# Optimization experiments

Hardware: AMD Instinct MI355X
Metric: run time of the kernel (lower is better)

## Reference

```python
import jax, jax.numpy as jnp
import numpy as np

N, D_IN, D_OUT = 2048, 256, 64
ALPHA = 0.2  # LeakyReLU slope
LN_EPS = 1e-5


def setup_inputs() -> dict:
    key = jax.random.key(0)
    ks = jax.random.split(key, 8)
    features = jax.random.normal(ks[0], (N, D_IN), dtype=jnp.float32)
    adj = jax.random.randint(ks[1], (N, N), 0, 2, dtype=jnp.int32)
    adj = adj.at[jnp.arange(N), jnp.arange(N)].set(1)  # self-loops: no all-masked rows
    s_in = 1.0 / np.sqrt(D_IN)
    s_out = 1.0 / np.sqrt(D_OUT)
    phi_w = jax.random.uniform(ks[2], (D_OUT, D_IN), jnp.float32, -s_in, s_in)
    phi_b = jax.random.uniform(ks[3], (D_OUT,), jnp.float32, -s_in, s_in)
    mu_w = jax.random.uniform(ks[4], (D_OUT,), jnp.float32, -s_out, s_out)
    mu_b = jax.random.uniform(ks[5], (), jnp.float32, -s_out, s_out)
    ln_g = jnp.ones((D_OUT,), jnp.float32)
    ln_b = jnp.zeros((D_OUT,), jnp.float32)
    return {"features": features, "adj": adj, "phi_w": phi_w, "phi_b": phi_b,
            "ln_g": ln_g, "ln_b": ln_b, "mu_w": mu_w, "mu_b": mu_b}


def _layernorm(x, g, b):
    mu = jnp.mean(x, axis=-1, keepdims=True)
    var = jnp.mean(jnp.square(x - mu), axis=-1, keepdims=True)
    return (x - mu) * jax.lax.rsqrt(var + LN_EPS) * g + b


def reference(features, adj, phi_w, phi_b, ln_g, ln_b, mu_w, mu_b):
    h = features @ phi_w.T + phi_b           # [N, D_OUT]
    h = _layernorm(h, ln_g, ln_b)
    # v2 path: scores[i,j,:] = h[i] + h[j]; e = mu(scores)
    scores = h[:, None, :] + h[None, :, :]   # [N, N, D_OUT]
    e = jnp.einsum('ijd,d->ij', scores, mu_w) + mu_b  # [N, N]
    e = jax.nn.leaky_relu(e, ALPHA)          # activation applied after if/else
    e = jnp.where(adj == 0, -jnp.inf, e)
    a = jax.nn.softmax(e, axis=1)            # dropout p=0 -> identity
    return jax.nn.elu(a @ h)                 # [N, D_OUT]
```

## Files before the change

kernel.cpp:

```cpp
#include <hip/hip_runtime.h>
#include <hip/hip_bf16.h>

#define N_ROWS 2048
#define D_IN   256
#define D_OUT  64
#define JSLAB  8
#define ALPHA  0.2f
#define LN_EPS 1e-5f

typedef __attribute__((ext_vector_type(4))) float f32x4;
typedef __attribute__((ext_vector_type(8))) short s16x8;

static __device__ __forceinline__ unsigned short f2bf(float x) {
    unsigned u = __float_as_uint(x);
    unsigned r = (u + 0x7FFFu + ((u >> 16) & 1u)) >> 16;
    return (unsigned short)r;
}
static __device__ __forceinline__ float bf2f(unsigned short u) {
    return __uint_as_float(((unsigned)u) << 16);
}

__global__ __launch_bounds__(256) void k1_h_s(
    const float* __restrict__ F, const float* __restrict__ phiW,
    const float* __restrict__ phiB, const float* __restrict__ lnG,
    const float* __restrict__ lnB, const float* __restrict__ muW,
    float* __restrict__ s_out, unsigned short* __restrict__ HhiT,
    unsigned short* __restrict__ HloT)
{
    __shared__ f32x4 phiS[64 * 64];
    __shared__ unsigned short Thi[64][8];
    __shared__ unsigned short Tlo[64][8];

    const int tid  = threadIdx.x;
    const int w    = tid >> 6;
    const int lane = tid & 63;
    const int i_base = blockIdx.x * 8;
    const int r0 = i_base + w * 2;

    const f32x4* phiW4 = (const f32x4*)phiW;
    const f32x4* F4    = (const f32x4*)F;

    #pragma unroll
    for (int t = 0; t < 16; ++t) {
        int idx = tid + t * 256;
        int d = idx >> 6, g = idx & 63;
        phiS[(d << 6) | (g ^ (d & 7))] = phiW4[idx];
    }
    __syncthreads();

    float acc[2] = {0.f, 0.f};
    for (int g = 0; g < 64; ++g) {
        f32x4 p = phiS[(lane << 6) | (g ^ (lane & 7))];
        #pragma unroll
        for (int rr = 0; rr < 2; ++rr) {
            f32x4 f = F4[(r0 + rr) * 64 + g];
            acc[rr] += p.x * f.x + p.y * f.y + p.z * f.z + p.w * f.w;
        }
    }

    const float pb = phiB[lane], gg = lnG[lane], bb = lnB[lane], mw = muW[lane];

    #pragma unroll
    for (int rr = 0; rr < 2; ++rr) {
        float h = acc[rr] + pb;
        float m = h;
        #pragma unroll
        for (int off = 32; off >= 1; off >>= 1) m += __shfl_xor(m, off);
        m *= (1.f / 64.f);
        float c = h - m;
        float v = c * c;
        #pragma unroll
        for (int off = 32; off >= 1; off >>= 1) v += __shfl_xor(v, off);
        v *= (1.f / 64.f);
        float hn = c * rsqrtf(v + LN_EPS) * gg + bb;
        float sp = hn * mw;
        #pragma unroll
        for (int off = 32; off >= 1; off >>= 1) sp += __shfl_xor(sp, off);
        if (lane == 0) s_out[r0 + rr] = sp;
        unsigned short hi = f2bf(hn);
        unsigned short lo = f2bf(hn - bf2f(hi));
        Thi[lane][w * 2 + rr] = hi;
        Tlo[lane][w * 2 + rr] = lo;
    }
    __syncthreads();
    if (tid < 128) {
        int d = tid >> 1, half = tid & 1;
        ushort4 vh = *(const ushort4*)&Thi[d][half * 4];
        *(ushort4*)&HhiT[d * N_ROWS + i_base + half * 4] = vh;
        ushort4 vl = *(const ushort4*)&Tlo[d][half * 4];
        *(ushort4*)&HloT[d * N_ROWS + i_base + half * 4] = vl;
    }
}

__global__ __launch_bounds__(256) void k2_attn(
    const int* __restrict__ adj, const float* __restrict__ s,
    const unsigned short* __restrict__ HhiT, const unsigned short* __restrict__ HloT,
    const float* __restrict__ muB,
    float* __restrict__ num_p, float* __restrict__ l_p)
{
    const int tid  = threadIdx.x;
    const int w    = tid >> 6;
    const int lane = tid & 63;
    const int stripe = blockIdx.x >> 3;
    const int slab   = blockIdx.x & (JSLAB - 1);
    const int i0 = stripe * 16;
    const int jb = slab * 256 + w * 64;
    const float mub = muB[0];

    __shared__ __align__(16) unsigned short Wt[4][16][72];
    __shared__ f32x4 cN[4][4][64];
    __shared__ f32x4 cL[4][64];

    const int rsel = lane & 15;
    const int rsub = lane >> 4;

    f32x4 accN[4];
    f32x4 accL;
    #pragma unroll
    for (int nb = 0; nb < 4; ++nb) { accN[nb][0]=0.f; accN[nb][1]=0.f; accN[nb][2]=0.f; accN[nb][3]=0.f; }
    accL[0]=0.f; accL[1]=0.f; accL[2]=0.f; accL[3]=0.f;

    s16x8 ones;
    #pragma unroll
    for (int e = 0; e < 8; ++e) ones[e] = (short)0x3F80;

    const float4 sj4 = ((const float4*)s)[(jb >> 2) + rsel];
    const int4* adj4 = (const int4*)adj;
    #pragma unroll
    for (int r4 = 0; r4 < 4; ++r4) {
        const int row = r4 * 4 + rsub;
        const int i = i0 + row;
        const float si = s[i];
        int4 a = adj4[(size_t)i * (N_ROWS / 4) + (jb >> 2) + rsel];
        ushort4 pk;
        {
            float z = si + sj4.x + mub; float e = z > 0.f ? z : ALPHA * z;
            pk.x = a.x ? f2bf(__expf(e)) : 0;
        }{
            float z = si + sj4.y + mub; float e = z > 0.f ? z : ALPHA * z;
            pk.y = a.y ? f2bf(__expf(e)) : 0;
        }{
            float z = si + sj4.z + mub; float e = z > 0.f ? z : ALPHA * z;
            pk.z = a.z ? f2bf(__expf(e)) : 0;
        }{
            float z = si + sj4.w + mub; float e = z > 0.f ? z : ALPHA * z;
            pk.w = a.w ? f2bf(__expf(e)) : 0;
        }
        *(ushort4*)&Wt[w][row][rsel * 4] = pk;
    }

    s16x8 a0 = *(const s16x8*)&Wt[w][rsel][rsub * 8];
    s16x8 a1 = *(const s16x8*)&Wt[w][rsel][32 + rsub * 8];

    accL = __builtin_amdgcn_mfma_f32_16x16x32_bf16(a0, ones, accL, 0, 0, 0);
    accL = __builtin_amdgcn_mfma_f32_16x16x32_bf16(a1, ones, accL, 0, 0, 0);
    #pragma unroll
    for (int nb = 0; nb < 4; ++nb) {
        const unsigned short* hr = HhiT + (size_t)(nb * 16 + rsel) * N_ROWS + jb + rsub * 8;
        s16x8 b0 = *(const s16x8*)hr;
        s16x8 b1 = *(const s16x8*)(hr + 32);
        accN[nb] = __builtin_amdgcn_mfma_f32_16x16x32_bf16(a0, b0, accN[nb], 0, 0, 0);
        accN[nb] = __builtin_amdgcn_mfma_f32_16x16x32_bf16(a1, b1, accN[nb], 0, 0, 0);
        const unsigned short* lr = HloT + (size_t)(nb * 16 + rsel) * N_ROWS + jb + rsub * 8;
        s16x8 c0 = *(const s16x8*)lr;
        s16x8 c1 = *(const s16x8*)(lr + 32);
        accN[nb] = __builtin_amdgcn_mfma_f32_16x16x32_bf16(a0, c0, accN[nb], 0, 0, 0);
        accN[nb] = __builtin_amdgcn_mfma_f32_16x16x32_bf16(a1, c1, accN[nb], 0, 0, 0);
    }

    #pragma unroll
    for (int nb = 0; nb < 4; ++nb) cN[w][nb][lane] = accN[nb];
    cL[w][lane] = accL;
    __syncthreads();

    {
        f32x4 n = cN[0][w][lane] + cN[1][w][lane] + cN[2][w][lane] + cN[3][w][lane];
        float* np = num_p + (size_t)slab * (N_ROWS * D_OUT);
        #pragma unroll
        for (int r = 0; r < 4; ++r)
            np[(i0 + rsub * 4 + r) * D_OUT + w * 16 + rsel] = n[r];
    }
    if (w == 0) {
        f32x4 l = cL[0][lane] + cL[1][lane] + cL[2][lane] + cL[3][lane];
        if (rsel == 0) {
            #pragma unroll
            for (int r = 0; r < 4; ++r)
                l_p[slab * N_ROWS + i0 + rsub * 4 + r] = l[r];
        }
    }
}

__global__ __launch_bounds__(256) void k3_combine(
    const float* __restrict__ num_p, const float* __restrict__ l_p,
    float* __restrict__ out)
{
    const int g = blockIdx.x * 256 + threadIdx.x;
    const int i = g >> 6;
    float num = 0.f, l = 0.f;
    #pragma unroll
    for (int js = 0; js < JSLAB; ++js) {
        num += num_p[(size_t)js * (N_ROWS * D_OUT) + g];
        l   += l_p[js * N_ROWS + i];
    }
    const float o = num / l;
    out[g] = o > 0.f ? o : expm1f(o);
}

extern "C" void kernel_launch(void* const* d_in, const int* in_sizes, int n_in,
                              void* d_out, int out_size, void* d_ws, size_t ws_size,
                              hipStream_t stream)
{
    const float* F    = (const float*)d_in[0];
    const int*   adj  = (const int*)d_in[1];
    const float* phiW = (const float*)d_in[2];
    const float* phiB = (const float*)d_in[3];
    const float* lnG  = (const float*)d_in[4];
    const float* lnB  = (const float*)d_in[5];
    const float* muW  = (const float*)d_in[6];
    const float* muB  = (const float*)d_in[7];
    float* out = (float*)d_out;

    float* ws   = (float*)d_ws;
    float* s    = ws;
    float* l_p  = ws + N_ROWS;
    float* numP = l_p + (size_t)JSLAB * N_ROWS;
    unsigned short* HhiT = (unsigned short*)(numP + (size_t)JSLAB * N_ROWS * D_OUT);
    unsigned short* HloT = HhiT + (size_t)D_OUT * N_ROWS;

    k1_h_s<<<dim3(N_ROWS / 8), dim3(256), 0, stream>>>(F, phiW, phiB, lnG, lnB, muW,
                                                       s, HhiT, HloT);
    k2_attn<<<dim3((N_ROWS / 16) * JSLAB), dim3(256), 0, stream>>>(adj, s, HhiT, HloT, muB,
                                                                   numP, l_p);
    k3_combine<<<dim3((N_ROWS * D_OUT) / 256), dim3(256), 0, stream>>>(numP, l_p, out);
}
```

Baseline: 27.13 us.

## Fuse three kernels into one persistent kernel with grid barrier and finisher combine

Merges the projection/LayerNorm kernel, the attention slab kernel and the combine kernel into one 512-block launch. A global atomic grid barrier separates phase one from phase two, and a per-stripe atomic counter lets the last block for each stripe do the final normalize and ELU. The aim is to remove two kernel launch gaps and the separate combine pass. In exchange it adds a memset launch and spin-wait barrier overhead, and it relies on all 512 blocks being co-resident (launch bounds of 2 blocks per CU); otherwise the barrier deadlocks.

```diff
diff --git a/kernel.cpp b/kernel.cpp
--- a/kernel.cpp
+++ b/kernel.cpp
@@ -5,6 +5,7 @@
 #define D_IN   256
 #define D_OUT  64
 #define JSLAB  8
+#define NBLK   512
 #define ALPHA  0.2f
 #define LN_EPS 1e-5f
 
@@ -20,49 +21,61 @@
     return __uint_as_float(((unsigned)u) << 16);
 }
 
-__global__ __launch_bounds__(256) void k1_h_s(
-    const float* __restrict__ F, const float* __restrict__ phiW,
-    const float* __restrict__ phiB, const float* __restrict__ lnG,
-    const float* __restrict__ lnB, const float* __restrict__ muW,
-    float* __restrict__ s_out, unsigned short* __restrict__ HhiT,
-    unsigned short* __restrict__ HloT)
+__global__ __launch_bounds__(256, 2) void fused_gat(
+    const float* __restrict__ F, const int* __restrict__ adj,
+    const float* __restrict__ phiW, const float* __restrict__ phiB,
+    const float* __restrict__ lnG, const float* __restrict__ lnB,
+    const float* __restrict__ muW, const float* __restrict__ muB,
+    int* __restrict__ bar,
+    float* __restrict__ s_buf, float* __restrict__ l_p,
+    float* __restrict__ numP, unsigned short* __restrict__ HhiT,
+    unsigned short* __restrict__ HloT, float* __restrict__ out)
 {
-    __shared__ f32x4 phiS[64 * 64];
-    __shared__ unsigned short Thi[64][8];
-    __shared__ unsigned short Tlo[64][8];
+    __shared__ union {
+        struct {
+            f32x4 phiS[64 * 32];
+            unsigned short Thi[64][4];
+            unsigned short Tlo[64][4];
+        } p1;
+        struct {
+            unsigned short Wt[4][16][72];
+            f32x4 cN[4][4][64];
+            f32x4 cL[4][64];
+        } p2;
+    } sm;
+    __shared__ int finisher;
 
     const int tid  = threadIdx.x;
     const int w    = tid >> 6;
     const int lane = tid & 63;
-    const int i_base = blockIdx.x * 8;
-    const int r0 = i_base + w * 2;
-
-    const f32x4* phiW4 = (const f32x4*)phiW;
-    const f32x4* F4    = (const f32x4*)F;
-
-    #pragma unroll
-    for (int t = 0; t < 16; ++t) {
-        int idx = tid + t * 256;
-        int d = idx >> 6, g = idx & 63;
-        phiS[(d << 6) | (g ^ (d & 7))] = phiW4[idx];
-    }
-    __syncthreads();
-
-    float acc[2] = {0.f, 0.f};
-    for (int g = 0; g < 64; ++g) {
-        f32x4 p = phiS[(lane << 6) | (g ^ (lane & 7))];
-        #pragma unroll
-        for (int rr = 0; rr < 2; ++rr) {
-            f32x4 f = F4[(r0 + rr) * 64 + g];
-            acc[rr] += p.x * f.x + p.y * f.y + p.z * f.z + p.w * f.w;
-        }
-    }
-
-    const float pb = phiB[lane], gg = lnG[lane], bb = lnB[lane], mw = muW[lane];
-
-    #pragma unroll
-    for (int rr = 0; rr < 2; ++rr) {
-        float h = acc[rr] + pb;
+    const int bid  = blockIdx.x;
+
+    {
+        const int r = bid * 4 + w;
+        const f32x4* phiW4 = (const f32x4*)phiW;
+        const f32x4* F4    = (const f32x4*)F;
+
+        float acc0 = 0.f, acc1 = 0.f;
+        for (int half = 0; half < 2; ++half) {
+            __syncthreads();
+            #pragma unroll
+            for (int t = 0; t < 8; ++t) {
+                int idx = tid + t * 256;
+                int d = idx >> 5, g = idx & 31;
+                sm.p1.phiS[(d << 5) | (g ^ (d & 7))] = phiW4[d * 64 + half * 32 + g];
+            }
+            __syncthreads();
+            #pragma unroll
+            for (int g = 0; g < 32; ++g) {
+                f32x4 p = sm.p1.phiS[(lane << 5) | (g ^ (lane & 7))];
+                f32x4 f = F4[r * 64 + half * 32 + g];
+                float d0 = p.x * f.x + p.y * f.y + p.z * f.z + p.w * f.w;
+                if (g & 1) acc1 += d0; else acc0 += d0;
+            }
+        }
+
+        const float pb = phiB[lane], gg = lnG[lane], bb = lnB[lane], mw = muW[lane];
+        float h = acc0 + acc1 + pb;
         float m = h;
         #pragma unroll
         for (int off = 32; off >= 1; off >>= 1) m += __shfl_xor(m, off);
@@ -76,134 +89,143 @@
         float sp = hn * mw;
         #pragma unroll
         for (int off = 32; off >= 1; off >>= 1) sp += __shfl_xor(sp, off);
-        if (lane == 0) s_out[r0 + rr] = sp;
+        if (lane == 0) s_buf[r] = sp;
         unsigned short hi = f2bf(hn);
         unsigned short lo = f2bf(hn - bf2f(hi));
-        Thi[lane][w * 2 + rr] = hi;
-        Tlo[lane][w * 2 + rr] = lo;
-    }
-    __syncthreads();
-    if (tid < 128) {
-        int d = tid >> 1, half = tid & 1;
-        ushort4 vh = *(const ushort4*)&Thi[d][half * 4];
-        *(ushort4*)&HhiT[d * N_ROWS + i_base + half * 4] = vh;
-        ushort4 vl = *(const ushort4*)&Tlo[d][half * 4];
-        *(ushort4*)&HloT[d * N_ROWS + i_base + half * 4] = vl;
-    }
-}
-
-__global__ __launch_bounds__(256) void k2_attn(
-    const int* __restrict__ adj, const float* __restrict__ s,
-    const unsigned short* __restrict__ HhiT, const unsigned short* __restrict__ HloT,
-    const float* __restrict__ muB,
-    float* __restrict__ num_p, float* __restrict__ l_p)
-{
-    const int tid  = threadIdx.x;
-    const int w    = tid >> 6;
-    const int lane = tid & 63;
-    const int stripe = blockIdx.x >> 3;
-    const int slab   = blockIdx.x & (JSLAB - 1);
+        sm.p1.Thi[lane][w] = hi;
+        sm.p1.Tlo[lane][w] = lo;
+        __syncthreads();
+        if (tid < 64) {
+            *(ushort4*)&HhiT[tid * N_ROWS + bid * 4] = *(const ushort4*)&sm.p1.Thi[tid][0];
+        } else if (tid < 128) {
+            int d = tid - 64;
+            *(ushort4*)&HloT[d * N_ROWS + bid * 4] = *(const ushort4*)&sm.p1.Tlo[d][0];
+        }
+    }
+
+    __syncthreads();
+    if (tid == 0) {
+        __threadfence();
+        atomicAdd(&bar[0], 1);
+        while (atomicAdd(&bar[0], 0) < NBLK) __builtin_amdgcn_s_sleep(1);
+        __threadfence();
+    }
+    __syncthreads();
+
+    const int stripe = bid >> 2;
     const int i0 = stripe * 16;
-    const int jb = slab * 256 + w * 64;
     const float mub = muB[0];
-
-    __shared__ __align__(16) unsigned short Wt[4][16][72];
-    __shared__ f32x4 cN[4][4][64];
-    __shared__ f32x4 cL[4][64];
-
     const int rsel = lane & 15;
     const int rsub = lane >> 4;
-
-    f32x4 accN[4];
-    f32x4 accL;
-    #pragma unroll
-    for (int nb = 0; nb < 4; ++nb) { accN[nb][0]=0.f; accN[nb][1]=0.f; accN[nb][2]=0.f; accN[nb][3]=0.f; }
-    accL[0]=0.f; accL[1]=0.f; accL[2]=0.f; accL[3]=0.f;
 
     s16x8 ones;
     #pragma unroll
     for (int e = 0; e < 8; ++e) ones[e] = (short)0x3F80;
 
-    const float4 sj4 = ((const float4*)s)[(jb >> 2) + rsel];
-    const int4* adj4 = (const int4*)adj;
     #pragma unroll
-    for (int r4 = 0; r4 < 4; ++r4) {
-        const int row = r4 * 4 + rsub;
-        const int i = i0 + row;
-        const float si = s[i];
-        int4 a = adj4[(size_t)i * (N_ROWS / 4) + (jb >> 2) + rsel];
-        ushort4 pk;
+    for (int t = 0; t < 2; ++t) {
+        const int slab = (bid * 2 + t) & 7;
+        const int jb = slab * 256 + w * 64;
+
+        f32x4 accN[4];
+        f32x4 accL;
+        #pragma unroll
+        for (int nb = 0; nb < 4; ++nb) { accN[nb][0]=0.f; accN[nb][1]=0.f; accN[nb][2]=0.f; accN[nb][3]=0.f; }
+        accL[0]=0.f; accL[1]=0.f; accL[2]=0.f; accL[3]=0.f;
+
+        __syncthreads();
+
+        const float4 sj4 = ((const float4*)s_buf)[(jb >> 2) + rsel];
+        const int4* adj4 = (const int4*)adj;
+        #pragma unroll
+        for (int r4 = 0; r4 < 4; ++r4) {
+            const int row = r4 * 4 + rsub;
+            const int i = i0 + row;
+            const float si = s_buf[i];
+            int4 a = adj4[(size_t)i * (N_ROWS / 4) + (jb >> 2) + rsel];
+            ushort4 pk;
+            { float z = si + sj4.x + mub; float e = z > 0.f ? z : ALPHA * z; pk.x = a.x ? f2bf(__expf(e)) : 0; }
+            { float z = si + sj4.y + mub; float e = z > 0.f ? z : ALPHA * z; pk.y = a.y ? f2bf(__expf(e)) : 0; }
+            { float z = si + sj4.z + mub; float e = z > 0.f ? z : ALPHA * z; pk.z = a.z ? f2bf(__expf(e)) : 0; }
+            { float z = si + sj4.w + mub; float e = z > 0.f ? z : ALPHA * z; pk.w = a.w ? f2bf(__expf(e)) : 0; }
+            *(ushort4*)&sm.p2.Wt[w][row][rsel * 4] = pk;
+        }
+
+        s16x8 a0 = *(const s16x8*)&sm.p2.Wt[w][rsel][rsub * 8];
+        s16x8 a1 = *(const s16x8*)&sm.p2.Wt[w][rsel][32 + rsub * 8];
+
+        accL = __builtin_amdgcn_mfma_f32_16x16x32_bf16(a0, ones, accL, 0, 0, 0);
+        accL = __builtin_amdgcn_mfma_f32_16x16x32_bf16(a1, ones, accL, 0, 0, 0);
+        #pragma unroll
+        for (int nb = 0; nb < 4; ++nb) {
+            const unsigned short* hr = HhiT + (size_t)(nb * 16 + rsel) * N_ROWS + jb + rsub * 8;
+            s16x8 b0 = *(const s16x8*)hr;
+            s16x8 b1 = *(const s16x8*)(hr + 32);
+            accN[nb] = __builtin_amdgcn_mfma_f32_16x16x32_bf16(a0, b0, accN[nb], 0, 0, 0);
+            accN[nb] = __builtin_amdgcn_mfma_f32_16x16x32_bf16(a1, b1, accN[nb], 0, 0, 0);
+            const unsigned short* lr = HloT + (size_t)(nb * 16 + rsel) * N_ROWS + jb + rsub * 8;
+            s16x8 c0 = *(const s16x8*)lr;
+            s16x8 c1 = *(const s16x8*)(lr + 32);
+            accN[nb] = __builtin_amdgcn_mfma_f32_16x16x32_bf16(a0, c0, accN[nb], 0, 0, 0);
+            accN[nb] = __builtin_amdgcn_mfma_f32_16x16x32_bf16(a1, c1, accN[nb], 0, 0, 0);
+        }
+
+        #pragma unroll
+        for (int nb = 0; nb < 4; ++nb) sm.p2.cN[w][nb][lane] = accN[nb];
+        sm.p2.cL[w][lane] = accL;
+        __syncthreads();
+
         {
-            float z = si + sj4.x + mub; float e = z > 0.f ? z : ALPHA * z;
-            pk.x = a.x ? f2bf(__expf(e)) : 0;
-        }{
-            float z = si + sj4.y + mub; float e = z > 0.f ? z : ALPHA * z;
-            pk.y = a.y ? f2bf(__expf(e)) : 0;
-        }{
-            float z = si + sj4.z + mub; float e = z > 0.f ? z : ALPHA * z;
-            pk.z = a.z ? f2bf(__expf(e)) : 0;
-        }{
-            float z = si + sj4.w + mub; float e = z > 0.f ? z : ALPHA * z;
-            pk.w = a.w ? f2bf(__expf(e)) : 0;
-        }
-        *(ushort4*)&Wt[w][row][rsel * 4] = pk;
-    }
-
-    s16x8 a0 = *(const s16x8*)&Wt[w][rsel][rsub * 8];
-    s16x8 a1 = *(const s16x8*)&Wt[w][rsel][32 + rsub * 8];
-
-    accL = __builtin_amdgcn_mfma_f32_16x16x32_bf16(a0, ones, accL, 0, 0, 0);
-    accL = __builtin_amdgcn_mfma_f32_16x16x32_bf16(a1, ones, accL, 0, 0, 0);
-    #pragma unroll
-    for (int nb = 0; nb < 4; ++nb) {
-        const unsigned short* hr = HhiT + (size_t)(nb * 16 + rsel) * N_ROWS + jb + rsub * 8;
-        s16x8 b0 = *(const s16x8*)hr;
-        s16x8 b1 = *(const s16x8*)(hr + 32);
-        accN[nb] = __builtin_amdgcn_mfma_f32_16x16x32_bf16(a0, b0, accN[nb], 0, 0, 0);
-        accN[nb] = __builtin_amdgcn_mfma_f32_16x16x32_bf16(a1, b1, accN[nb], 0, 0, 0);
-        const unsigned short* lr = HloT + (size_t)(nb * 16 + rsel) * N_ROWS + jb + rsub * 8;
-        s16x8 c0 = *(const s16x8*)lr;
-        s16x8 c1 = *(const s16x8*)(lr + 32);
-        accN[nb] = __builtin_amdgcn_mfma_f32_16x16x32_bf16(a0, c0, accN[nb], 0, 0, 0);
-        accN[nb] = __builtin_amdgcn_mfma_f32_16x16x32_bf16(a1, c1, accN[nb], 0, 0, 0);
-    }
-
-    #pragma unroll
-    for (int nb = 0; nb < 4; ++nb) cN[w][nb][lane] = accN[nb];
-    cL[w][lane] = accL;
-    __syncthreads();
-
-    {
-        f32x4 n = cN[0][w][lane] + cN[1][w][lane] + cN[2][w][lane] + cN[3][w][lane];
-        float* np = num_p + (size_t)slab * (N_ROWS * D_OUT);
-        #pragma unroll
-        for (int r = 0; r < 4; ++r)
-            np[(i0 + rsub * 4 + r) * D_OUT + w * 16 + rsel] = n[r];
-    }
-    if (w == 0) {
-        f32x4 l = cL[0][lane] + cL[1][lane] + cL[2][lane] + cL[3][lane];
-        if (rsel == 0) {
+            f32x4 n = sm.p2.cN[0][w][lane] + sm.p2.cN[1][w][lane]
+                    + sm.p2.cN[2][w][lane] + sm.p2.cN[3][w][lane];
+            float* np = numP + (size_t)slab * (N_ROWS * D_OUT);
             #pragma unroll
             for (int r = 0; r < 4; ++r)
-                l_p[slab * N_ROWS + i0 + rsub * 4 + r] = l[r];
-        }
-    }
-}
-
-__global__ __launch_bounds__(256) void k3_combine(
-    const float* __restrict__ num_p, const float* __restrict__ l_p,
-    float* __restrict__ out)
-{
-    const int g = blockIdx.x * 256 + threadIdx.x;
-    const int i = g >> 6;
-    float num = 0.f, l = 0.f;
-    #pragma unroll
-    for (int js = 0; js < JSLAB; ++js) {
-        num += num_p[(size_t)js * (N_ROWS * D_OUT) + g];
-        l   += l_p[js * N_ROWS + i];
-    }
-    const float o = num / l;
-    out[g] = o > 0.f ? o : expm1f(o);
+                np[(i0 + rsub * 4 + r) * D_OUT + w * 16 + rsel] = n[r];
+        }
+        if (w == 0) {
+            f32x4 l = sm.p2.cL[0][lane] + sm.p2.cL[1][lane]
+                    + sm.p2.cL[2][lane] + sm.p2.cL[3][lane];
+            if (rsel == 0) {
+                #pragma unroll
+                for (int r = 0; r < 4; ++r)
+                    l_p[slab * N_ROWS + i0 + rsub * 4 + r] = l[r];
+            }
+        }
+    }
+
+    __syncthreads();
+    if (tid == 0) {
+        __threadfence();
+        int old = atomicAdd(&bar[1 + stripe], 1);
+        finisher = (old == 3);
+        if (old == 3) __threadfence();
+    }
+    __syncthreads();
+
+    if (finisher) {
+        const int idx = tid * 4;
+        const int r = idx >> 6;
+        const int c = idx & 63;
+        const int row = i0 + r;
+        f32x4 n = {0.f, 0.f, 0.f, 0.f};
+        float l = 0.f;
+        #pragma unroll
+        for (int sl = 0; sl < JSLAB; ++sl) {
+            const f32x4* np = (const f32x4*)(numP + (size_t)sl * (N_ROWS * D_OUT)
+                                             + row * D_OUT + c);
+            n += *np;
+            l += l_p[sl * N_ROWS + row];
+        }
+        const float inv = 1.f / l;
+        f32x4 o;
+        #pragma unroll
+        for (int e = 0; e < 4; ++e) {
+            float v = n[e] * inv;
+            o[e] = v > 0.f ? v : expm1f(v);
+        }
+        *(f32x4*)&out[row * D_OUT + c] = o;
+    }
 }
 
 extern "C" void kernel_launch(void* const* d_in, const int* in_sizes, int n_in,
@@ -220,16 +242,17 @@
     const float* muB  = (const float*)d_in[7];
     float* out = (float*)d_out;
 
-    float* ws   = (float*)d_ws;
+    int*   bar  = (int*)d_ws;
+    float* ws   = (float*)d_ws + 256;
     float* s    = ws;
     float* l_p  = ws + N_ROWS;
     float* numP = l_p + (size_t)JSLAB * N_ROWS;
     unsigned short* HhiT = (unsigned short*)(numP + (size_t)JSLAB * N_ROWS * D_OUT);
     unsigned short* HloT = HhiT + (size_t)D_OUT * N_ROWS;
 
-    k1_h_s<<<dim3(N_ROWS / 8), dim3(256), 0, stream>>>(F, phiW, phiB, lnG, lnB, muW,
-                                                       s, HhiT, HloT);
-    k2_attn<<<dim3((N_ROWS / 16) * JSLAB), dim3(256), 0, stream>>>(adj, s, HhiT, HloT, muB,
-                                                                   numP, l_p);
-    k3_combine<<<dim3((N_ROWS * D_OUT) / 256), dim3(256), 0, stream>>>(numP, l_p, out);
-}
+    hipMemsetAsync(bar, 0, 256 * sizeof(int), stream);
+
+    fused_gat<<<dim3(NBLK), dim3(256), 0, stream>>>(
+        F, adj, phiW, phiB, lnG, lnB, muW, muB,
+        bar, s, l_p, numP, HhiT, HloT, out);
+}
```

After: 106.8 us. +293.6%, slower.
